# Kernel tuning notes

Measured on AMD Instinct MI355X. Metric: run time of the kernel, lower is better.

The kernel has to match this reference:

```python
import jax, jax.numpy as jnp
import numpy as np

MARGIN = 1.0
EPS = 1e-6  # torch F.pairwise_distance default eps, added elementwise to (x - y)
NEG_INF = -1e30
POS_INF = 1e30


def _pairwise_dist_matrix(e):
    # D[i,j] = || e_i - e_j + EPS ||_2, expanded so we never materialize [B,B,D]:
    # ||d + eps||^2 = ||d||^2 + 2*eps*sum(d) + Dfeat*eps^2,  d = e_i - e_j
    sq = jnp.sum(e * e, axis=1)          # [B]
    s = jnp.sum(e, axis=1)               # [B]
    d2 = (sq[:, None] + sq[None, :] - 2.0 * (e @ e.T)
          + 2.0 * EPS * (s[:, None] - s[None, :])
          + e.shape[1] * (EPS * EPS))
    return jnp.sqrt(jnp.maximum(d2, 0.0))  # [B,B]


def _pdist(x, y):
    # F.pairwise_distance(p=2): ||x - y + eps||
    return jnp.sqrt(jnp.sum(jnp.square(x - y + EPS), axis=-1))


def setup_inputs() -> dict:
    B, D = 4096, 128
    key = jax.random.key(0)
    k1, k2, k3, k4 = jax.random.split(key, 4)
    embedding = jax.random.normal(k1, (B, D), dtype=jnp.float32)
    # label space == batch, each label appears exactly once in the batch
    target_idx = jax.random.permutation(k2, B).astype(jnp.int32)
    positive_idxs = jax.random.bernoulli(k3, 0.02, (B, B))  # [B, L] label-space mask
    negative_idxs = jax.random.bernoulli(k4, 0.5, (B, B))
    return {"embedding": embedding, "target_idx": target_idx,
            "positive_idxs": positive_idxs, "negative_idxs": negative_idxs}


def reference(embedding, target_idx, positive_idxs, negative_idxs):
    # Mining happens under no_grad in the original module.
    dm = jax.lax.stop_gradient(_pairwise_dist_matrix(embedding))  # [B,B]
    # batch j is a positive/negative candidate for anchor i iff its label is flagged
    pos_mask = positive_idxs[:, target_idx]  # [B,B] bool
    neg_mask = negative_idxs[:, target_idx]
    pos_idx = jnp.argmax(jnp.where(pos_mask, dm, NEG_INF), axis=1)  # hardest positive
    neg_idx = jnp.argmin(jnp.where(neg_mask, dm, POS_INF), axis=1)  # hardest negative
    valid = jnp.any(pos_mask, axis=1) & jnp.any(neg_mask, axis=1)
    a = embedding
    p = embedding[pos_idx]
    n = embedding[neg_idx]
    ap = _pdist(a, p)
    an = _pdist(a, n)
    pn = _pdist(p, n)
    loss = jax.nn.relu(ap - jnp.minimum(an, pn) + MARGIN)
    w = valid.astype(loss.dtype)
    return jnp.sum(loss * w) / jnp.maximum(jnp.sum(w), 1.0)
```

## Files before the change

### kernel.cpp

```cpp
#include <hip/hip_runtime.h>
#include <stdint.h>

#define BN 4096
#define DD 128
#define EPSF 1e-6f
#define MARGINF 1.0f

typedef unsigned long long ull;
typedef unsigned short ushort;
typedef short short8 __attribute__((ext_vector_type(8)));
typedef float f32x4 __attribute__((ext_vector_type(4)));

__device__ __forceinline__ unsigned int ord_f32(float f) {
    unsigned int u = __float_as_uint(f);
    return (u & 0x80000000u) ? ~u : (u | 0x80000000u);
}
__device__ __forceinline__ ushort bf16_rne(float x) {
    unsigned int u = __float_as_uint(x);
    return (ushort)((u + 0x7FFFu + ((u >> 16) & 1u)) >> 16);
}

__global__ void k_prep(const float* __restrict__ e, const int* __restrict__ tidx,
                       float* __restrict__ sq, float* __restrict__ s,
                       int* __restrict__ inv, ull* __restrict__ pk, ull* __restrict__ nk,
                       unsigned int* __restrict__ ehi) {
    int w = threadIdx.x >> 6, lane = threadIdx.x & 63;
    int row = blockIdx.x * 4 + w;
    float2 v = ((const float2*)(e + (size_t)row * DD))[lane];
    ushort hx = bf16_rne(v.x), hy = bf16_rne(v.y);
    ehi[row * 64 + lane] = (unsigned int)hx | ((unsigned int)hy << 16);
    float ss = v.x + v.y;
    float qq = v.x * v.x + v.y * v.y;
    #pragma unroll
    for (int off = 32; off > 0; off >>= 1) {
        ss += __shfl_down(ss, off);
        qq += __shfl_down(qq, off);
    }
    if (lane == 0) {
        sq[row] = qq; s[row] = ss;
        inv[tidx[row]] = row;
        pk[row] = 0ULL; nk[row] = 0ULL;
    }
}

__global__ void k_bits(const int* __restrict__ pos, const int* __restrict__ neg,
                       ushort* __restrict__ pb, ushort* __restrict__ nb) {
    const int row = blockIdx.x, t = threadIdx.x;
    const int4* pr = (const int4*)(pos + (size_t)row * BN) + t * 4;
    const int4* nr = (const int4*)(neg + (size_t)row * BN) + t * 4;
    int4 p0 = pr[0], p1 = pr[1], p2 = pr[2], p3 = pr[3];
    int4 n0 = nr[0], n1 = nr[1], n2 = nr[2], n3 = nr[3];
    unsigned int m = 0;
    m |= (p0.x != 0) << 0;  m |= (p0.y != 0) << 1;  m |= (p0.z != 0) << 2;  m |= (p0.w != 0) << 3;
    m |= (p1.x != 0) << 4;  m |= (p1.y != 0) << 5;  m |= (p1.z != 0) << 6;  m |= (p1.w != 0) << 7;
    m |= (p2.x != 0) << 8;  m |= (p2.y != 0) << 9;  m |= (p2.z != 0) << 10; m |= (p2.w != 0) << 11;
    m |= (p3.x != 0) << 12; m |= (p3.y != 0) << 13; m |= (p3.z != 0) << 14; m |= (p3.w != 0) << 15;
    pb[(size_t)row * 256 + t] = (ushort)m;
    m = 0;
    m |= (n0.x != 0) << 0;  m |= (n0.y != 0) << 1;  m |= (n0.z != 0) << 2;  m |= (n0.w != 0) << 3;
    m |= (n1.x != 0) << 4;  m |= (n1.y != 0) << 5;  m |= (n1.z != 0) << 6;  m |= (n1.w != 0) << 7;
    m |= (n2.x != 0) << 8;  m |= (n2.y != 0) << 9;  m |= (n2.z != 0) << 10; m |= (n2.w != 0) << 11;
    m |= (n3.x != 0) << 12; m |= (n3.y != 0) << 13; m |= (n3.z != 0) << 14; m |= (n3.w != 0) << 15;
    nb[(size_t)row * 256 + t] = (ushort)m;
}

__global__ __launch_bounds__(256, 4)
void k_select(const ushort* __restrict__ ehi,
              const float* __restrict__ sq, const float* __restrict__ s,
              const int* __restrict__ inv,
              const ull* __restrict__ pbits, const ull* __restrict__ nbits,
              ull* __restrict__ pkey, ull* __restrict__ nkey) {
    __shared__ __align__(16) char smem[36864];
    __shared__ float rjl[128];
    __shared__ int jvs[128];

    ushort* Bst = (ushort*)smem;

    const int tid = threadIdx.x;
    const int lane = tid & 63;
    const int w = tid >> 6, wr = w >> 1, wc = w & 1;
    const int lrow = lane & 15, quad = lane >> 4;
    const int i0 = blockIdx.x * 128, c0 = blockIdx.y * 128;

    if (tid < 128) {
        int j = inv[c0 + tid];
        jvs[tid] = j;
        rjl[tid] = sq[j] - 2.0f * EPSF * s[j];
    }
    __syncthreads();

    #pragma unroll
    for (int it = 0; it < 8; it++) {
        int slot = it * 256 + tid;
        int r = slot >> 4, seg16 = slot & 15;
        int kc = seg16 >> 3, seg = seg16 & 7;
        int jr = jvs[r];
        int4 v = ((const int4*)ehi)[(size_t)jr * 16 + seg16];
        *(int4*)(Bst + (kc * 128 + r) * 72 + seg * 8) = v;
    }
    __syncthreads();

    f32x4 acc[4][4];
    #pragma unroll
    for (int rt = 0; rt < 4; rt++)
        #pragma unroll
        for (int ct = 0; ct < 4; ct++)
            acc[rt][ct] = (f32x4){0.f, 0.f, 0.f, 0.f};

    size_t abase[4];
    #pragma unroll
    for (int rt = 0; rt < 4; rt++)
        abase[rt] = (size_t)(i0 + wr * 64 + rt * 16 + lrow) * DD + quad * 8;

    #pragma unroll
    for (int ks = 0; ks < 4; ks++) {
        const int kc = ks >> 1, ksl = ks & 1;
        short8 ah[4];
        #pragma unroll
        for (int rt = 0; rt < 4; rt++)
            ah[rt] = *(const short8*)(ehi + abase[rt] + ks * 32);
        #pragma unroll
        for (int ct = 0; ct < 4; ct++) {
            const int bo = (kc * 128 + wc * 64 + ct * 16 + lrow) * 72 + ksl * 32 + quad * 8;
            short8 bh = *(const short8*)(Bst + bo);
            #pragma unroll
            for (int rt = 0; rt < 4; rt++)
                acc[rt][ct] = __builtin_amdgcn_mfma_f32_16x16x32_bf16(ah[rt], bh, acc[rt][ct], 0, 0, 0);
        }
    }

    __syncthreads();
    ull* pbl = (ull*)smem;
    ull* nbl = (ull*)(smem + 2048);
    {
        int r = tid >> 1, h = tid & 1;
        size_t b = (size_t)(i0 + r) * 64 + (c0 >> 6) + h;
        pbl[tid] = pbits[b];
        nbl[tid] = nbits[b];
    }
    __syncthreads();

    int jcol[4]; float rjc[4];
    #pragma unroll
    for (int ct = 0; ct < 4; ct++) {
        jcol[ct] = jvs[wc * 64 + ct * 16 + lrow];
        rjc[ct] = rjl[wc * 64 + ct * 16 + lrow];
    }
    ull* scrp = (ull*)(smem + 4096);
    ull* scrn = (ull*)(smem + 20480);
    #pragma unroll
    for (int rt = 0; rt < 4; rt++)
        #pragma unroll
        for (int t = 0; t < 4; t++) {
            const int row = wr * 64 + rt * 16 + quad * 4 + t;
            ull pb = pbl[row * 2 + wc] >> lrow;
            ull nb = nbl[row * 2 + wc] >> lrow;
            float bpv = -3.4e38f, bnv = 3.4e38f;
            int bpi = 0x7FFFFFFF, bni = 0x7FFFFFFF;
            #pragma unroll
            for (int ct = 0; ct < 4; ct++) {
                float m = rjc[ct] - 2.0f * acc[rt][ct][t];
                int j = jcol[ct];
                if ((pb >> (ct * 16)) & 1ULL) {
                    if (m > bpv || (m == bpv && j < bpi)) { bpv = m; bpi = j; }
                }
                if ((nb >> (ct * 16)) & 1ULL) {
                    if (m < bnv || (m == bnv && j < bni)) { bnv = m; bni = j; }
                }
            }
            ull kp = (bpi == 0x7FFFFFFF) ? 0ULL
                   : (((ull)ord_f32(bpv) << 32) | (ull)(0xFFFFFFFFu - (unsigned)bpi));
            ull kn = (bni == 0x7FFFFFFF) ? 0ULL
                   : (((ull)(~ord_f32(bnv)) << 32) | (ull)(0xFFFFFFFFu - (unsigned)bni));
            ull op = __shfl_xor(kp, 8); if (op > kp) kp = op;
            ull on = __shfl_xor(kn, 8); if (on > kn) kn = on;
            if (lrow < 8) {
                scrp[(wc * 8 + lrow) * 128 + row] = kp;
                scrn[(wc * 8 + lrow) * 128 + row] = kn;
            }
        }
    __syncthreads();
    if (tid < 128) {
        ull kp = 0ULL, kn = 0ULL;
        #pragma unroll
        for (int k = 0; k < 16; k++) {
            ull v = scrp[k * 128 + tid]; if (v > kp) kp = v;
            v = scrn[k * 128 + tid];     if (v > kn) kn = v;
        }
        if (kp) atomicMax(&pkey[i0 + tid], kp);
        if (kn) atomicMax(&nkey[i0 + tid], kn);
    }
}

__global__ void k_loss(const float* __restrict__ e,
                       const ull* __restrict__ pkey, const ull* __restrict__ nkey,
                       float* __restrict__ partials) {
    int w = threadIdx.x >> 6, lane = threadIdx.x & 63;
    int row = blockIdx.x * 4 + w;
    ull pk = pkey[row], nk = nkey[row];
    float loss = 0.0f, wt = 0.0f;
    if (pk != 0ULL && nk != 0ULL) {
        int pi = (int)(0xFFFFFFFFu - (unsigned)(pk & 0xFFFFFFFFu));
        int ni = (int)(0xFFFFFFFFu - (unsigned)(nk & 0xFFFFFFFFu));
        float2 av = ((const float2*)(e + (size_t)row * DD))[lane];
        float2 pv = ((const float2*)(e + (size_t)pi * DD))[lane];
        float2 nv = ((const float2*)(e + (size_t)ni * DD))[lane];
        float dx, dy;
        dx = av.x - pv.x + EPSF; dy = av.y - pv.y + EPSF;
        float ap2 = dx * dx + dy * dy;
        dx = av.x - nv.x + EPSF; dy = av.y - nv.y + EPSF;
        float an2 = dx * dx + dy * dy;
        dx = pv.x - nv.x + EPSF; dy = pv.y - nv.y + EPSF;
        float pn2 = dx * dx + dy * dy;
        #pragma unroll
        for (int off = 32; off > 0; off >>= 1) {
            ap2 += __shfl_down(ap2, off);
            an2 += __shfl_down(an2, off);
            pn2 += __shfl_down(pn2, off);
        }
        if (lane == 0) {
            float ap = sqrtf(ap2), an = sqrtf(an2), pn = sqrtf(pn2);
            loss = fmaxf(ap - fminf(an, pn) + MARGINF, 0.0f);
            wt = 1.0f;
        }
    }
    __shared__ float sl[4], sw[4];
    if (lane == 0) { sl[w] = loss; sw[w] = wt; }
    __syncthreads();
    if (threadIdx.x == 0) {
        partials[blockIdx.x * 2 + 0] = sl[0] + sl[1] + sl[2] + sl[3];
        partials[blockIdx.x * 2 + 1] = sw[0] + sw[1] + sw[2] + sw[3];
    }
}

__global__ void k_final(const float* __restrict__ partials, float* __restrict__ out) {
    int tid = threadIdx.x;
    float L = 0.0f, W = 0.0f;
    for (int i = 0; i < 4; i++) {
        int idx = tid + i * 256;
        L += partials[idx * 2];
        W += partials[idx * 2 + 1];
    }
    #pragma unroll
    for (int off = 32; off > 0; off >>= 1) {
        L += __shfl_down(L, off);
        W += __shfl_down(W, off);
    }
    __shared__ float sl[4], sw[4];
    int w = tid >> 6, lane = tid & 63;
    if (lane == 0) { sl[w] = L; sw[w] = W; }
    __syncthreads();
    if (tid == 0) {
        float Lt = sl[0] + sl[1] + sl[2] + sl[3];
        float Wt = sw[0] + sw[1] + sw[2] + sw[3];
        out[0] = Lt / fmaxf(Wt, 1.0f);
    }
}

extern "C" void kernel_launch(void* const* d_in, const int* in_sizes, int n_in,
                              void* d_out, int out_size, void* d_ws, size_t ws_size,
                              hipStream_t stream) {
    const float* e    = (const float*)d_in[0];
    const int*   tidx = (const int*)d_in[1];
    const int*   pos  = (const int*)d_in[2];
    const int*   neg  = (const int*)d_in[3];
    float* out = (float*)d_out;

    ull* pkey  = (ull*)d_ws;
    ull* nkey  = pkey + BN;
    ull* pbits = nkey + BN;
    ull* nbits = pbits + BN * 64;
    float* sq  = (float*)(nbits + BN * 64);
    float* s   = sq + BN;
    int* inv   = (int*)(s + BN);
    float* partials = (float*)(inv + BN);
    unsigned int* ehi = (unsigned int*)(partials + 2048);

    k_prep<<<BN / 4, 256, 0, stream>>>(e, tidx, sq, s, inv, pkey, nkey, ehi);
    k_bits<<<BN, 256, 0, stream>>>(pos, neg, (ushort*)pbits, (ushort*)nbits);
    dim3 grid(BN / 128, BN / 128);
    k_select<<<grid, 256, 0, stream>>>((const ushort*)ehi, sq, s, inv,
                                       pbits, nbits, pkey, nkey);
    k_loss<<<BN / 4, 256, 0, stream>>>(e, pkey, nkey, partials);
    k_final<<<1, 256, 0, stream>>>(partials, out);
}
```

Baseline: 185.7 us.

## Fuse mask bit-packing into selection kernel, dropping separate k_bits pass

Removes the standalone k_bits kernel and has each k_select block read its 128x128 tile of the int32 positive/negative masks directly, turning them into nibbles in shared memory and then packing them into 64-bit words. This avoids a kernel launch and the write and reread of the packed bitmask buffers in global memory. Each block now does 16 strided int4 loads per thread per mask before the MFMA stage, which may add latency at block start unless other resident blocks hide it.

Measured after the change: 184.4 us (median of 2 runs). About the same (-0.7%).

```diff
diff --git a/kernel.cpp b/kernel.cpp
--- a/kernel.cpp
+++ b/kernel.cpp
@@ -18,6 +18,13 @@
 __device__ __forceinline__ ushort bf16_rne(float x) {
     unsigned int u = __float_as_uint(x);
     return (ushort)((u + 0x7FFFu + ((u >> 16) & 1u)) >> 16);
+}
+__device__ __forceinline__ unsigned int pack8(ull v) {
+    v &= 0x0F0F0F0F0F0F0F0FULL;
+    v = (v | (v >> 4)) & 0x00FF00FF00FF00FFULL;
+    v = (v | (v >> 8)) & 0x0000FFFF0000FFFFULL;
+    v = (v | (v >> 16));
+    return (unsigned int)v;
 }
 
 __global__ void k_prep(const float* __restrict__ e, const int* __restrict__ tidx,
@@ -43,38 +50,15 @@
     }
 }
 
-__global__ void k_bits(const int* __restrict__ pos, const int* __restrict__ neg,
-                       ushort* __restrict__ pb, ushort* __restrict__ nb) {
-    const int row = blockIdx.x, t = threadIdx.x;
-    const int4* pr = (const int4*)(pos + (size_t)row * BN) + t * 4;
-    const int4* nr = (const int4*)(neg + (size_t)row * BN) + t * 4;
-    int4 p0 = pr[0], p1 = pr[1], p2 = pr[2], p3 = pr[3];
-    int4 n0 = nr[0], n1 = nr[1], n2 = nr[2], n3 = nr[3];
-    unsigned int m = 0;
-    m |= (p0.x != 0) << 0;  m |= (p0.y != 0) << 1;  m |= (p0.z != 0) << 2;  m |= (p0.w != 0) << 3;
-    m |= (p1.x != 0) << 4;  m |= (p1.y != 0) << 5;  m |= (p1.z != 0) << 6;  m |= (p1.w != 0) << 7;
-    m |= (p2.x != 0) << 8;  m |= (p2.y != 0) << 9;  m |= (p2.z != 0) << 10; m |= (p2.w != 0) << 11;
-    m |= (p3.x != 0) << 12; m |= (p3.y != 0) << 13; m |= (p3.z != 0) << 14; m |= (p3.w != 0) << 15;
-    pb[(size_t)row * 256 + t] = (ushort)m;
-    m = 0;
-    m |= (n0.x != 0) << 0;  m |= (n0.y != 0) << 1;  m |= (n0.z != 0) << 2;  m |= (n0.w != 0) << 3;
-    m |= (n1.x != 0) << 4;  m |= (n1.y != 0) << 5;  m |= (n1.z != 0) << 6;  m |= (n1.w != 0) << 7;
-    m |= (n2.x != 0) << 8;  m |= (n2.y != 0) << 9;  m |= (n2.z != 0) << 10; m |= (n2.w != 0) << 11;
-    m |= (n3.x != 0) << 12; m |= (n3.y != 0) << 13; m |= (n3.z != 0) << 14; m |= (n3.w != 0) << 15;
-    nb[(size_t)row * 256 + t] = (ushort)m;
-}
-
 __global__ __launch_bounds__(256, 4)
 void k_select(const ushort* __restrict__ ehi,
+              const int* __restrict__ pos, const int* __restrict__ neg,
               const float* __restrict__ sq, const float* __restrict__ s,
               const int* __restrict__ inv,
-              const ull* __restrict__ pbits, const ull* __restrict__ nbits,
               ull* __restrict__ pkey, ull* __restrict__ nkey) {
     __shared__ __align__(16) char smem[36864];
     __shared__ float rjl[128];
     __shared__ int jvs[128];
-
-    ushort* Bst = (ushort*)smem;
 
     const int tid = threadIdx.x;
     const int lane = tid & 63;
@@ -87,8 +71,42 @@
         jvs[tid] = j;
         rjl[tid] = sq[j] - 2.0f * EPSF * s[j];
     }
-    __syncthreads();
-
+
+    unsigned char* nibP = (unsigned char*)smem;
+    unsigned char* nibN = (unsigned char*)(smem + 4096);
+    {
+        const int4* pbase = (const int4*)(pos + (size_t)i0 * BN + c0);
+        const int4* nbase = (const int4*)(neg + (size_t)i0 * BN + c0);
+        #pragma unroll
+        for (int p = 0; p < 16; p++) {
+            int flat = p * 256 + tid;
+            int r = flat >> 5, q = flat & 31;
+            size_t idx = (size_t)r * (BN / 4) + q;
+            int4 P = pbase[idx];
+            int4 N = nbase[idx];
+            unsigned int pm = (unsigned int)(P.x != 0) | ((unsigned int)(P.y != 0) << 1)
+                            | ((unsigned int)(P.z != 0) << 2) | ((unsigned int)(P.w != 0) << 3);
+            unsigned int nm = (unsigned int)(N.x != 0) | ((unsigned int)(N.y != 0) << 1)
+                            | ((unsigned int)(N.z != 0) << 2) | ((unsigned int)(N.w != 0) << 3);
+            nibP[r * 32 + q] = (unsigned char)pm;
+            nibN[r * 32 + q] = (unsigned char)nm;
+        }
+    }
+    __syncthreads();
+
+    ull pw, nw;
+    {
+        int off = (tid >> 1) * 32 + (tid & 1) * 16;
+        ull lo = *(const ull*)(nibP + off);
+        ull hi = *(const ull*)(nibP + off + 8);
+        pw = (ull)pack8(lo) | ((ull)pack8(hi) << 32);
+        lo = *(const ull*)(nibN + off);
+        hi = *(const ull*)(nibN + off + 8);
+        nw = (ull)pack8(lo) | ((ull)pack8(hi) << 32);
+    }
+    __syncthreads();
+
+    ushort* Bst = (ushort*)smem;
     #pragma unroll
     for (int it = 0; it < 8; it++) {
         int slot = it * 256 + tid;
@@ -132,12 +150,8 @@
     __syncthreads();
     ull* pbl = (ull*)smem;
     ull* nbl = (ull*)(smem + 2048);
-    {
-        int r = tid >> 1, h = tid & 1;
-        size_t b = (size_t)(i0 + r) * 64 + (c0 >> 6) + h;
-        pbl[tid] = pbits[b];
-        nbl[tid] = nbits[b];
-    }
+    pbl[tid] = pw;
+    nbl[tid] = nw;
     __syncthreads();
 
     int jcol[4]; float rjc[4];
@@ -268,19 +282,16 @@
 
     ull* pkey  = (ull*)d_ws;
     ull* nkey  = pkey + BN;
-    ull* pbits = nkey + BN;
-    ull* nbits = pbits + BN * 64;
-    float* sq  = (float*)(nbits + BN * 64);
+    float* sq  = (float*)(nkey + BN);
     float* s   = sq + BN;
     int* inv   = (int*)(s + BN);
     float* partials = (float*)(inv + BN);
     unsigned int* ehi = (unsigned int*)(partials + 2048);
 
     k_prep<<<BN / 4, 256, 0, stream>>>(e, tidx, sq, s, inv, pkey, nkey, ehi);
-    k_bits<<<BN, 256, 0, stream>>>(pos, neg, (ushort*)pbits, (ushort*)nbits);
     dim3 grid(BN / 128, BN / 128);
-    k_select<<<grid, 256, 0, stream>>>((const ushort*)ehi, sq, s, inv,
-                                       pbits, nbits, pkey, nkey);
+    k_select<<<grid, 256, 0, stream>>>((const ushort*)ehi, pos, neg,
+                                       sq, s, inv, pkey, nkey);
     k_loss<<<BN / 4, 256, 0, stream>>>(e, pkey, nkey, partials);
     k_final<<<1, 256, 0, stream>>>(partials, out);
 }
```
